# Optimization experiments

Hardware: AMD Instinct MI355X
Metric: run time of the kernel (lower is better)

Reference implementation:

```python
import math
import jax, jax.numpy as jnp
import numpy as np

B, S, D_IN, D_OUT = 8, 4096, 512, 512
CHUNK = 64
MAX_LR = 0.2        # config.max_memory_lr
MIN_DECAY = 0.5     # config.min_memory_decay
MAX_NORM = 30.0     # config.memory_max_norm
NORM_EPS = 1e-5     # config.norm_eps (used in normalize_for_delta)


def setup_inputs() -> dict:
    key = jax.random.key(0)
    ks = jax.random.split(key, 5)
    x = jax.random.normal(ks[0], (B, S, D_IN), dtype=jnp.float32)
    # M_init: xavier_uniform(gain=0.1) ~ small; use small normal
    M_init = jax.random.normal(ks[1], (D_OUT, D_IN), dtype=jnp.float32) * 0.02
    # hyperparam projections (Linear(d_in, 1)); torch init: zero weight, logit bias.
    # Use small random weights so the data-dependent path is exercised.
    eta_w = jax.random.normal(ks[2], (1, D_IN), dtype=jnp.float32) * 0.01
    eta_b = jnp.full((1,), math.log(0.08 / 0.92), dtype=jnp.float32)   # inv_sig(memory_lr_init)
    alpha_w = jax.random.normal(ks[3], (1, D_IN), dtype=jnp.float32) * 0.01
    alpha_b = jnp.full((1,), math.log(0.85 / 0.15), dtype=jnp.float32)  # inv_sig(memory_decay_init)
    gate_w = jax.random.normal(ks[4], (1, D_IN), dtype=jnp.float32) * 0.01
    gate_b = jnp.full((1,), 2.0, dtype=jnp.float32)
    return {"x": x, "M_init": M_init, "eta_w": eta_w, "eta_b": eta_b,
            "alpha_w": alpha_w, "alpha_b": alpha_b, "gate_w": gate_w, "gate_b": gate_b}


def _forward(x, M_init, eta_w, eta_b, alpha_w, alpha_b, gate_w, gate_b):
    n_chunks = S // CHUNK
    # [n_chunks, B, C, d_in] for scan over chunks
    xc = x.reshape(B, n_chunks, CHUNK, D_IN).transpose(1, 0, 2, 3)
    M0 = jnp.broadcast_to(M_init, (B, D_OUT, D_IN))

    def step(M, chunk):  # M: [B, d_out, d_in], chunk: [B, C, d_in]
        # per-chunk hyperparams (training mode: base logits = 0)
        eta_tok = jax.nn.sigmoid(chunk @ eta_w.T + eta_b) * MAX_LR            # [B,C,1]
        alpha_tok = MIN_DECAY + jax.nn.sigmoid(chunk @ alpha_w.T + alpha_b) * (1.0 - MIN_DECAY)
        eta = eta_tok.mean(axis=1, keepdims=True)    # [B,1,1]
        alpha = alpha_tok.mean(axis=1, keepdims=True)
        # retrieval: chunk @ M^T
        outputs = jnp.einsum('bcd,bod->bco', chunk, M)  # [B,C,d_out]
        # normalized keys (F.normalize: x / max(||x||, eps))
        kn = jnp.linalg.norm(chunk, axis=-1, keepdims=True)
        keys = chunk / jnp.maximum(kn, NORM_EPS)
        k_mean = keys.mean(axis=1)        # [B,d_in]
        v_target = outputs.mean(axis=1)   # [B,d_out]
        # delta rule rank-1 update
        Mk = jnp.einsum('bod,bd->bo', M, k_mean)
        error = v_target - Mk
        update = error[:, :, None] * k_mean[:, None, :]  # [B,d_out,d_in]
        # chunk_scale = min(C/chunk_size, 1) = 1 here
        M_new = alpha * M + eta * update
        gate = jax.nn.sigmoid(k_mean @ gate_w.T + gate_b)[:, :, None]  # [B,1,1]
        M_new = gate * M_new + (1.0 - gate) * M
        # frobenius-norm clamp
        M_norm = jnp.sqrt(jnp.sum(M_new * M_new, axis=(-2, -1), keepdims=True))
        scale = jnp.minimum(MAX_NORM / (M_norm + 1e-6), 1.0)
        return M_new * scale, outputs

    M_fin, outs = jax.lax.scan(step, M0, xc)  # outs: [n_chunks,B,C,d_out]
    out = outs.transpose(1, 0, 2, 3).reshape(B, S, D_OUT)
    return out, M_fin


def reference(x, M_init, eta_w, eta_b, alpha_w, alpha_b, gate_w, gate_b):
    return _forward(x, M_init, eta_w, eta_b, alpha_w, alpha_b, gate_w, gate_b)
```

## Files before the change

kernel.cpp:

```cpp
#include <hip/hip_runtime.h>
#include <math.h>

#define DIN  512
#define DOUT 512
#define CHK  64
#define NCH  64
#define NB   8
#define SEQ  4096

typedef short bh8_t __attribute__((ext_vector_type(8)));
typedef float f32x4 __attribute__((ext_vector_type(4)));

__device__ __forceinline__ float sigmoidf_(float z){ return 1.0f/(1.0f+__expf(-z)); }

__device__ __forceinline__ unsigned short f2bf(float f){
  unsigned u = __float_as_uint(f);
  unsigned r = (u + 0x7fffu + ((u>>16)&1u)) >> 16;
  return (unsigned short)r;
}
__device__ __forceinline__ void store_bf4(unsigned short* p, float4 v){
  uint2 u;
  u.x = (unsigned)f2bf(v.x) | ((unsigned)f2bf(v.y)<<16);
  u.y = (unsigned)f2bf(v.z) | ((unsigned)f2bf(v.w)<<16);
  *(uint2*)p = u;
}

__global__ __launch_bounds__(256) void k0_m0h(const float* __restrict__ M0, unsigned short* __restrict__ M0h){
  int idx = (blockIdx.x*256 + threadIdx.x)*4;
  float4 v = *(const float4*)(M0+idx);
  store_bf4(M0h+idx, v);
}

__global__ __launch_bounds__(256) void k1_stats(
    const float* __restrict__ x,
    const float* __restrict__ eta_w, const float* __restrict__ eta_b,
    const float* __restrict__ alpha_w, const float* __restrict__ alpha_b,
    const float* __restrict__ gate_w, const float* __restrict__ gate_b,
    float* __restrict__ KM, float* __restrict__ Dv, unsigned short* __restrict__ KMh,
    float* __restrict__ C1, float* __restrict__ C2, float* __restrict__ KM2, float* __restrict__ Q,
    unsigned short* __restrict__ xh)
{
  int j = blockIdx.x, b = blockIdx.y;
  const float* xc = x + ((size_t)b*SEQ + (size_t)j*CHK) * DIN;
  int tid = threadIdx.x;
  int wave = tid >> 6, lane = tid & 63;

  float km_acc[8], xb_acc[8];
#pragma unroll
  for (int k=0;k<8;k++){ km_acc[k]=0.f; xb_acc[k]=0.f; }
  float eta_sum = 0.f, alpha_sum = 0.f;
  float ew[8], aw[8];
#pragma unroll
  for (int k=0;k<8;k++){ ew[k]=eta_w[lane*8+k]; aw[k]=alpha_w[lane*8+k]; }

  for (int tt=0; tt<16; tt++){
    int t = wave*16 + tt;
    const float* xr = xc + (size_t)t*DIN + lane*8;
    float v[8];
#pragma unroll
    for (int k=0;k<8;k++) v[k]=xr[k];
    if (xh){
      uint4 hv;
      hv.x = (unsigned)f2bf(v[0]) | ((unsigned)f2bf(v[1])<<16);
      hv.y = (unsigned)f2bf(v[2]) | ((unsigned)f2bf(v[3])<<16);
      hv.z = (unsigned)f2bf(v[4]) | ((unsigned)f2bf(v[5])<<16);
      hv.w = (unsigned)f2bf(v[6]) | ((unsigned)f2bf(v[7])<<16);
      *(uint4*)&xh[((size_t)b*SEQ + (size_t)j*CHK + t)*DIN + lane*8] = hv;
    }
    float pe=0.f, pa=0.f, pn=0.f;
#pragma unroll
    for (int k=0;k<8;k++){ pe += v[k]*ew[k]; pa += v[k]*aw[k]; pn += v[k]*v[k]; }
#pragma unroll
    for (int off=32; off; off>>=1){
      pe += __shfl_xor(pe, off);
      pa += __shfl_xor(pa, off);
      pn += __shfl_xor(pn, off);
    }
    float inv = 1.0f / fmaxf(sqrtf(pn), 1e-5f);
    eta_sum   += sigmoidf_(pe + eta_b[0]);
    alpha_sum += sigmoidf_(pa + alpha_b[0]);
#pragma unroll
    for (int k=0;k<8;k++){ km_acc[k] += v[k]*inv; xb_acc[k] += v[k]; }
  }

  __shared__ float sKM[4][DIN];
  __shared__ float sXB[4][DIN];
  __shared__ float sEA[4][2];
  __shared__ float sred[4][2];
#pragma unroll
  for (int k=0;k<8;k++){ sKM[wave][lane*8+k]=km_acc[k]; sXB[wave][lane*8+k]=xb_acc[k]; }
  if (lane==0){ sEA[wave][0]=eta_sum; sEA[wave][1]=alpha_sum; }
  __syncthreads();

  float gpart=0.f, km2part=0.f;
  float kmv[2], dvv[2];
#pragma unroll
  for (int k=0;k<2;k++){
    int d = tid*2+k;
    float km = (sKM[0][d]+sKM[1][d]+sKM[2][d]+sKM[3][d]) * (1.0f/64.0f);
    float xb = (sXB[0][d]+sXB[1][d]+sXB[2][d]+sXB[3][d]) * (1.0f/64.0f);
    kmv[k]=km; dvv[k]=xb-km;
    gpart  += km * gate_w[d];
    km2part+= km * km;
  }
#pragma unroll
  for (int off=32; off; off>>=1){
    gpart   += __shfl_xor(gpart, off);
    km2part += __shfl_xor(km2part, off);
  }
  if (lane==0){ sred[wave][0]=gpart; sred[wave][1]=km2part; }
  __syncthreads();

  size_t base = ((size_t)b*NCH + j)*DIN;
#pragma unroll
  for (int k=0;k<2;k++){
    int d = tid*2+k;
    KM[base+d]=kmv[k];
    Dv[base+d]=dvv[k];
    KMh[base+d]=f2bf(kmv[k]);
  }
  if (tid==0){
    float gdot = sred[0][0]+sred[1][0]+sred[2][0]+sred[3][0];
    float km2  = sred[0][1]+sred[1][1]+sred[2][1]+sred[3][1];
    float etam = (sEA[0][0]+sEA[1][0]+sEA[2][0]+sEA[3][0]) * (1.0f/64.0f);
    float alpm = (sEA[0][1]+sEA[1][1]+sEA[2][1]+sEA[3][1]) * (1.0f/64.0f);
    float eta   = 0.2f * etam;
    float alpha = 0.5f + 0.5f * alpm;
    float gate  = sigmoidf_(gdot + gate_b[0]);
    float c1 = gate*alpha + 1.0f - gate;
    float c2 = gate*eta;
    C1[b*NCH+j]  = c1;
    C2[b*NCH+j]  = c2;
    KM2[b*NCH+j] = km2;
    Q[b*NCH+j]   = c2/c1;
  }
}

__global__ __launch_bounds__(256) void k2_g0h0(
    const float* __restrict__ KM, const float* __restrict__ Dv,
    const float* __restrict__ M0, float* __restrict__ G0, float* __restrict__ H0)
{
  int j = blockIdx.x, b = blockIdx.y;
  __shared__ float sD[DIN], sK[DIN];
  int tid = threadIdx.x;
  size_t base = ((size_t)b*NCH+j)*DIN;
  for (int d=tid; d<DIN; d+=256){ sD[d]=Dv[base+d]; sK[d]=KM[base+d]; }
  __syncthreads();
  for (int o=tid; o<DOUT; o+=256){
    const float* mr = M0 + (size_t)o*DIN;
    float ag=0.f, ah=0.f;
    for (int d=0; d<DIN; d+=4){
      float4 m = *(const float4*)(mr+d);
      ag += m.x*sD[d] + m.y*sD[d+1] + m.z*sD[d+2] + m.w*sD[d+3];
      ah += m.x*sK[d] + m.y*sK[d+1] + m.z*sK[d+2] + m.w*sK[d+3];
    }
    G0[base+o]=ag; H0[base+o]=ah;
  }
}

__global__ __launch_bounds__(256) void k2b_gram(
    const float* __restrict__ KM, const float* __restrict__ Dv,
    float* __restrict__ KMD, float* __restrict__ KMKM)
{
  int i = blockIdx.x, b = blockIdx.y;
  __shared__ float sKi[DIN];
  int tid = threadIdx.x;
  const float* kmi = KM + ((size_t)b*NCH+i)*DIN;
  for (int d=tid; d<DIN; d+=256) sKi[d]=kmi[d];
  __syncthreads();
  int wave = tid>>6, lane = tid&63;
  for (int j=wave; j<NCH; j+=4){
    const float* dj = Dv + ((size_t)b*NCH+j)*DIN;
    const float* kj = KM + ((size_t)b*NCH+j)*DIN;
    float pd=0.f, pk=0.f;
#pragma unroll
    for (int k=0;k<8;k++){
      int d = lane + k*64;
      pd += sKi[d]*dj[d];
      pk += sKi[d]*kj[d];
    }
#pragma unroll
    for (int off=32; off; off>>=1){ pd += __shfl_xor(pd,off); pk += __shfl_xor(pk,off); }
    if (lane==0){
      KMD [((size_t)b*NCH+i)*NCH + j] = pd;
      KMKM[((size_t)b*NCH+i)*NCH + j] = pk;
    }
  }
}

__global__ __launch_bounds__(256) void k3a_au(
    const float* __restrict__ G0, const float* __restrict__ H0,
    const float* __restrict__ KMD, const float* __restrict__ KMKM,
    const float* __restrict__ Q, float* __restrict__ AU,
    unsigned short* __restrict__ UQTh,
    float* __restrict__ DUW, float* __restrict__ DUU)
{
  int half = blockIdx.x, b = blockIdx.y;
  int tid = threadIdx.x, wave = tid>>6, lane = tid&63;
  int d = half*256 + tid;
  __shared__ float scM[4096], scW[4096];
  __shared__ float sq[64];
  __shared__ float sdots[64][4][2];

  for (int idx=tid; idx<4096; idx+=256){
    int i=idx>>6, jj=idx&63;
    float qv = Q[b*NCH+i];
    scM[idx] = qv*KMD [((size_t)b*NCH+i)*NCH+jj];
    scW[idx] = qv*KMKM[((size_t)b*NCH+i)*NCH+jj];
  }
  if (tid<64) sq[tid] = Q[b*NCH+tid];
  __syncthreads();

  float au[NCH];
  size_t gb = (size_t)b*NCH*DOUT + d;
#pragma unroll
  for (int j=0;j<NCH;j++) au[j] = G0[gb + (size_t)j*DOUT];

#pragma unroll
  for (int j=0;j<NCH;j++){
    float a = au[j];
#pragma unroll
    for (int i=0;i<j;i++) a += scM[i*64+j]*au[i];
    au[j]=a;
  }
#pragma unroll
  for (int j=0;j<NCH;j++) AU[gb + (size_t)j*DOUT] = au[j];

#pragma unroll
  for (int g=0; g<8; g++){
    uint4 hv;
    hv.x = (unsigned)f2bf(au[g*8+0]*sq[g*8+0]) | ((unsigned)f2bf(au[g*8+1]*sq[g*8+1])<<16);
    hv.y = (unsigned)f2bf(au[g*8+2]*sq[g*8+2]) | ((unsigned)f2bf(au[g*8+3]*sq[g*8+3])<<16);
    hv.z = (unsigned)f2bf(au[g*8+4]*sq[g*8+4]) | ((unsigned)f2bf(au[g*8+5]*sq[g*8+5])<<16);
    hv.w = (unsigned)f2bf(au[g*8+6]*sq[g*8+6]) | ((unsigned)f2bf(au[g*8+7]*sq[g*8+7])<<16);
    *(uint4*)&UQTh[((size_t)b*DOUT + d)*NCH + g*8] = hv;
  }

#pragma unroll
  for (int j=0;j<NCH;j++){
    float w = H0[gb + (size_t)j*DOUT];
#pragma unroll
    for (int i=0;i<j;i++) w += scW[i*64+j]*au[i];
    float s1 = au[j]*w, s2 = au[j]*au[j];
#pragma unroll
    for (int off=32; off; off>>=1){ s1+=__shfl_xor(s1,off); s2+=__shfl_xor(s2,off); }
    if (lane==0){ sdots[j][wave][0]=s1; sdots[j][wave][1]=s2; }
  }
  __syncthreads();
  if (tid<64){
    int j = tid;
    float uw = sdots[j][0][0]+sdots[j][1][0]+sdots[j][2][0]+sdots[j][3][0];
    float uu = sdots[j][0][1]+sdots[j][1][1]+sdots[j][2][1]+sdots[j][3][1];
    DUW[(b*NCH+j)*2 + half] = uw;
    DUU[(b*NCH+j)*2 + half] = uu;
  }
}

__global__ __launch_bounds__(256) void k3c_chain(
    const float* __restrict__ M0,
    const float* __restrict__ C1, const float* __restrict__ C2, const float* __restrict__ KM2,
    const float* __restrict__ DUW, const float* __restrict__ DUU, float* __restrict__ P)
{
  int b = blockIdx.x, tid = threadIdx.x, wave = tid>>6, lane = tid&63;
  float f=0.f;
  const float4* m4 = (const float4*)M0;
  for (int i=tid; i<(DOUT*DIN)/4; i+=256){
    float4 v=m4[i];
    f += v.x*v.x + v.y*v.y + v.z*v.z + v.w*v.w;
  }
#pragma unroll
  for (int off=32; off; off>>=1) f += __shfl_xor(f,off);
  __shared__ float rf[4];
  if (lane==0) rf[wave]=f;
  __syncthreads();
  if (tid==0){
    float F = rf[0]+rf[1]+rf[2]+rf[3];
    float p = 1.f;
    P[b*65+0] = 1.f;
    for (int j=0;j<NCH;j++){
      float c1 = C1[b*NCH+j], c2 = C2[b*NCH+j], km2 = KM2[b*NCH+j];
      float uw = p*p*(DUW[(b*NCH+j)*2]+DUW[(b*NCH+j)*2+1]);
      float uu = p*p*(DUU[(b*NCH+j)*2]+DUU[(b*NCH+j)*2+1]);
      float Fnew = c1*c1*F + 2.f*c1*c2*uw + c2*c2*uu*km2;
      float scale = fminf(30.0f/(sqrtf(Fnew)+1e-6f), 1.0f);
      F = scale*scale*Fnew;
      p = scale*c1*p;
      P[b*65+j+1] = p;
    }
  }
}

__global__ __launch_bounds__(256) void k4s_s(
    const float* __restrict__ x, const unsigned short* __restrict__ xh,
    const unsigned short* __restrict__ KMh,
    unsigned short* __restrict__ Sh, int use_xh)
{
  int tt = blockIdx.x, b = blockIdx.y;
  int tid = threadIdx.x;
  int lane = tid&63, w = tid>>6, m = lane&15, q = lane>>4;
  __shared__ unsigned short As[64*72];
  __shared__ unsigned short Bs[64*72];
  f32x4 acc[4];
  f32x4 z = {0.f,0.f,0.f,0.f};
#pragma unroll
  for (int nf=0;nf<4;nf++) acc[nf]=z;

  for (int k0=0;k0<DIN;k0+=64){
    uint4 bb[2];
#pragma unroll
    for (int v=0;v<2;v++){
      int idx=v*256+tid; int il=idx>>3, cc=idx&7;
      bb[v] = *(const uint4*)&KMh[((size_t)b*NCH+il)*DIN + k0 + cc*8];
    }
    if (use_xh){
      uint4 av[2];
#pragma unroll
      for (int v=0;v<2;v++){
        int idx=v*256+tid; int row=idx>>3, cc=idx&7;
        av[v] = *(const uint4*)&xh[((size_t)b*SEQ + (size_t)tt*64 + row)*DIN + k0 + cc*8];
      }
      __syncthreads();
#pragma unroll
      for (int v=0;v<2;v++){
        int idx=v*256+tid; int row=idx>>3, cc=idx&7;
        *(uint4*)&As[row*72 + cc*8] = av[v];
      }
    } else {
      float4 xa[4];
#pragma unroll
      for (int v=0;v<4;v++){
        int idx=v*256+tid; int row=idx>>4, cc=idx&15;
        xa[v] = *(const float4*)(x + ((size_t)b*SEQ + (size_t)tt*64 + row)*DIN + k0 + cc*4);
      }
      __syncthreads();
#pragma unroll
      for (int v=0;v<4;v++){
        int idx=v*256+tid; int row=idx>>4, cc=idx&15;
        store_bf4(&As[row*72 + cc*4], xa[v]);
      }
    }
#pragma unroll
    for (int v=0;v<2;v++){
      int idx=v*256+tid; int il=idx>>3, cc=idx&7;
      *(uint4*)&Bs[il*72 + cc*8] = bb[v];
    }
    __syncthreads();
#pragma unroll
    for (int kk=0;kk<2;kk++){
      bh8_t af = *(bh8_t*)&As[(w*16+m)*72 + kk*32 + q*8];
#pragma unroll
      for (int nf=0;nf<4;nf++){
        bh8_t bf_ = *(bh8_t*)&Bs[(nf*16+m)*72 + kk*32 + q*8];
        acc[nf] = __builtin_amdgcn_mfma_f32_16x16x32_bf16(af, bf_, acc[nf], 0,0,0);
      }
    }
  }
#pragma unroll
  for (int nf=0;nf<4;nf++)
#pragma unroll
    for (int r=0;r<4;r++)
      Sh[((size_t)b*SEQ + (size_t)tt*64 + w*16 + q*4 + r)*NCH + nf*16 + m] = f2bf(acc[nf][r]);
}

__global__ __launch_bounds__(256) void k4_out(
    const float* __restrict__ x, const unsigned short* __restrict__ xh,
    const unsigned short* __restrict__ M0h,
    const unsigned short* __restrict__ Sh, const unsigned short* __restrict__ UQTh,
    const float* __restrict__ P, float* __restrict__ out, int use_xh)
{
  int ot = blockIdx.x, j = blockIdx.y, b = blockIdx.z;
  int tid = threadIdx.x;
  int lane = tid&63, w = tid>>6, m = lane&15, q = lane>>4;
  int O0 = ot*256;
  __shared__ unsigned short As[64*72];
  __shared__ unsigned short Bs[256*72];
  f32x4 acc[16];
  f32x4 z = {0.f,0.f,0.f,0.f};
#pragma unroll
  for (int nf=0;nf<16;nf++) acc[nf]=z;

  for (int idx=tid; idx<64*64; idx+=256){
    int t = idx>>6, i = idx&63;
    As[t*72+i] = (i<j) ? Sh[((size_t)b*SEQ + (size_t)j*64 + t)*NCH + i] : (unsigned short)0;
  }
#pragma unroll
  for (int v=0; v<8; v++){
    int idx = v*256+tid;
    int ol = idx>>3, cc = idx&7;
    *(uint4*)&Bs[ol*72 + cc*8] = *(const uint4*)&UQTh[((size_t)b*DOUT + O0+ol)*NCH + cc*8];
  }
  __syncthreads();
#pragma unroll
  for (int kk=0;kk<2;kk++){
    bh8_t af = *(bh8_t*)&As[(w*16+m)*72 + kk*32 + q*8];
#pragma unroll
    for (int nf=0;nf<16;nf++){
      bh8_t bf_ = *(bh8_t*)&Bs[(nf*16+m)*72 + kk*32 + q*8];
      acc[nf] = __builtin_amdgcn_mfma_f32_16x16x32_bf16(af, bf_, acc[nf], 0,0,0);
    }
  }

  for (int k0=0;k0<DIN;k0+=64){
    uint4 bb[8];
#pragma unroll
    for (int v=0;v<8;v++){
      int idx=v*256+tid; int ol=idx>>3, cc=idx&7;
      bb[v] = *(const uint4*)&M0h[(size_t)(O0+ol)*DIN + k0 + cc*8];
    }
    if (use_xh){
      uint4 av[2];
#pragma unroll
      for (int v=0;v<2;v++){
        int idx=v*256+tid; int row=idx>>3, cc=idx&7;
        av[v] = *(const uint4*)&xh[((size_t)b*SEQ + (size_t)j*64 + row)*DIN + k0 + cc*8];
      }
      __syncthreads();
#pragma unroll
      for (int v=0;v<2;v++){
        int idx=v*256+tid; int row=idx>>3, cc=idx&7;
        *(uint4*)&As[row*72 + cc*8] = av[v];
      }
    } else {
      float4 xa[4];
#pragma unroll
      for (int v=0;v<4;v++){
        int idx=v*256+tid; int row=idx>>4, cc=idx&15;
        xa[v] = *(const float4*)(x + ((size_t)b*SEQ + (size_t)j*64 + row)*DIN + k0 + cc*4);
      }
      __syncthreads();
#pragma unroll
      for (int v=0;v<4;v++){
        int idx=v*256+tid; int row=idx>>4, cc=idx&15;
        store_bf4(&As[row*72 + cc*4], xa[v]);
      }
    }
#pragma unroll
    for (int v=0;v<8;v++){
      int idx=v*256+tid; int ol=idx>>3, cc=idx&7;
      *(uint4*)&Bs[ol*72 + cc*8] = bb[v];
    }
    __syncthreads();
#pragma unroll
    for (int kk=0;kk<2;kk++){
      bh8_t af = *(bh8_t*)&As[(w*16+m)*72 + kk*32 + q*8];
#pragma unroll
      for (int nf=0;nf<16;nf++){
        bh8_t bf_ = *(bh8_t*)&Bs[(nf*16+m)*72 + kk*32 + q*8];
        acc[nf] = __builtin_amdgcn_mfma_f32_16x16x32_bf16(af, bf_, acc[nf], 0,0,0);
      }
    }
  }

  float p = P[b*65 + j];
#pragma unroll
  for (int nf=0;nf<16;nf++)
#pragma unroll
    for (int r=0;r<4;r++)
      out[((size_t)b*SEQ + (size_t)j*64 + w*16 + q*4 + r)*DOUT + O0 + nf*16 + m] = p*acc[nf][r];
}

__global__ __launch_bounds__(256) void k5_mfin(
    const float* __restrict__ M0, const float* __restrict__ KM,
    const float* __restrict__ AU, const float* __restrict__ P, const float* __restrict__ Q,
    float* __restrict__ Mout)
{
  int ob = blockIdx.x, b = blockIdx.y;
  int tid = threadIdx.x;
  __shared__ float uo[64][8];
  for (int idx=tid; idx<512; idx+=256){
    int i = idx>>3, oo = idx&7;
    uo[i][oo] = Q[b*NCH+i] * AU[((size_t)b*NCH+i)*DOUT + ob*8+oo];
  }
  __syncthreads();
  float p64 = P[b*65+NCH];
  float acc[2][8];
#pragma unroll
  for (int h=0;h<2;h++)
#pragma unroll
    for (int oo=0;oo<8;oo++) acc[h][oo]=0.f;
  int d0 = tid, d1 = tid+256;
  for (int i=0;i<64;i++){
    float k0 = KM[((size_t)b*NCH+i)*DIN + d0];
    float k1 = KM[((size_t)b*NCH+i)*DIN + d1];
#pragma unroll
    for (int oo=0;oo<8;oo++){
      float u = uo[i][oo];
      acc[0][oo] += u*k0;
      acc[1][oo] += u*k1;
    }
  }
#pragma unroll
  for (int oo=0;oo<8;oo++){
    int o = ob*8+oo;
    Mout[((size_t)b*DOUT + o)*DIN + d0] = p64*(M0[(size_t)o*DIN+d0] + acc[0][oo]);
    Mout[((size_t)b*DOUT + o)*DIN + d1] = p64*(M0[(size_t)o*DIN+d1] + acc[1][oo]);
  }
}

extern "C" void kernel_launch(void* const* d_in, const int* in_sizes, int n_in,
                              void* d_out, int out_size, void* d_ws, size_t ws_size,
                              hipStream_t stream) {
  const float* x       = (const float*)d_in[0];
  const float* M0      = (const float*)d_in[1];
  const float* eta_w   = (const float*)d_in[2];
  const float* eta_b   = (const float*)d_in[3];
  const float* alpha_w = (const float*)d_in[4];
  const float* alpha_b = (const float*)d_in[5];
  const float* gate_w  = (const float*)d_in[6];
  const float* gate_b  = (const float*)d_in[7];
  float* out = (float*)d_out;

  float* ws = (float*)d_ws;
  float* KM   = ws;
  float* Dv   = KM   + 262144;
  float* G0   = Dv   + 262144;
  float* H0   = G0   + 262144;
  float* AU   = H0   + 262144;
  float* KMD  = AU   + 262144;
  float* KMKM = KMD  + 32768;
  float* C1   = KMKM + 32768;
  float* C2   = C1   + 512;
  float* KM2  = C2   + 512;
  float* Q    = KM2  + 512;
  float* DUW  = Q    + 512;
  float* DUU  = DUW  + 1024;
  float* P    = DUU  + 1024;
  unsigned short* M0h  = (unsigned short*)(P + 1024);
  unsigned short* KMh  = M0h  + 262144;
  unsigned short* Sh   = KMh  + 262144;
  unsigned short* UQTh = Sh   + 2097152;
  unsigned short* xh   = UQTh + 262144;

  size_t base_bytes = (size_t)((char*)xh - (char*)d_ws);
  size_t need_xh = base_bytes + (size_t)16777216*2;
  int use_xh = (ws_size >= need_xh) ? 1 : 0;
  unsigned short* xh_arg = use_xh ? xh : (unsigned short*)0;

  k0_m0h<<<dim3(256), 256, 0, stream>>>(M0, M0h);
  k1_stats<<<dim3(NCH, NB), 256, 0, stream>>>(x, eta_w, eta_b, alpha_w, alpha_b,
                                              gate_w, gate_b, KM, Dv, KMh, C1, C2, KM2, Q, xh_arg);
  k2_g0h0<<<dim3(NCH, NB), 256, 0, stream>>>(KM, Dv, M0, G0, H0);
  k2b_gram<<<dim3(NCH, NB), 256, 0, stream>>>(KM, Dv, KMD, KMKM);
  k4s_s<<<dim3(SEQ/64, NB), 256, 0, stream>>>(x, xh, KMh, Sh, use_xh);
  k3a_au<<<dim3(2, NB), 256, 0, stream>>>(G0, H0, KMD, KMKM, Q, AU, UQTh, DUW, DUU);
  k3c_chain<<<dim3(NB), 256, 0, stream>>>(M0, C1, C2, KM2, DUW, DUU, P);
  k4_out<<<dim3(2, NCH, NB), 256, 0, stream>>>(x, xh, M0h, Sh, UQTh, P, out, use_xh);
  k5_mfin<<<dim3(64, NB), 256, 0, stream>>>(M0, KM, AU, P, Q, out + (size_t)NB*SEQ*DOUT);
}
```

Measured before the change: 511.4 us.

## Fuse triangular solve with norm chain, split GEMM tiles, stage stores via LDS

The AU triangular solve and the scalar norm-chain kernel are merged into one 512-thread block per batch, which drops the DUW/DUU round trip and one launch. k2_g0h0 gets twice as many blocks (one per output half), and k2b_gram moves to 512 threads. k4_out halves its output tile to 128 columns so the grid doubles, and it stages results through LDS for coalesced float4 stores; k4s_s stages its bf16 stores the same way. The risk is that fewer blocks in the fused solve lengthen that serial step, and the smaller output tiles reload the A operand more often.

```diff
diff --git a/kernel.cpp b/kernel.cpp
--- a/kernel.cpp
+++ b/kernel.cpp
@@ -140,25 +140,24 @@
     const float* __restrict__ KM, const float* __restrict__ Dv,
     const float* __restrict__ M0, float* __restrict__ G0, float* __restrict__ H0)
 {
-  int j = blockIdx.x, b = blockIdx.y;
+  int j = blockIdx.x, b = blockIdx.y, half = blockIdx.z;
   __shared__ float sD[DIN], sK[DIN];
   int tid = threadIdx.x;
   size_t base = ((size_t)b*NCH+j)*DIN;
   for (int d=tid; d<DIN; d+=256){ sD[d]=Dv[base+d]; sK[d]=KM[base+d]; }
   __syncthreads();
-  for (int o=tid; o<DOUT; o+=256){
-    const float* mr = M0 + (size_t)o*DIN;
-    float ag=0.f, ah=0.f;
-    for (int d=0; d<DIN; d+=4){
-      float4 m = *(const float4*)(mr+d);
-      ag += m.x*sD[d] + m.y*sD[d+1] + m.z*sD[d+2] + m.w*sD[d+3];
-      ah += m.x*sK[d] + m.y*sK[d+1] + m.z*sK[d+2] + m.w*sK[d+3];
-    }
-    G0[base+o]=ag; H0[base+o]=ah;
-  }
-}
-
-__global__ __launch_bounds__(256) void k2b_gram(
+  int o = half*256 + tid;
+  const float* mr = M0 + (size_t)o*DIN;
+  float ag=0.f, ah=0.f;
+  for (int d=0; d<DIN; d+=4){
+    float4 m = *(const float4*)(mr+d);
+    ag += m.x*sD[d] + m.y*sD[d+1] + m.z*sD[d+2] + m.w*sD[d+3];
+    ah += m.x*sK[d] + m.y*sK[d+1] + m.z*sK[d+2] + m.w*sK[d+3];
+  }
+  G0[base+o]=ag; H0[base+o]=ah;
+}
+
+__global__ __launch_bounds__(512) void k2b_gram(
     const float* __restrict__ KM, const float* __restrict__ Dv,
     float* __restrict__ KMD, float* __restrict__ KMKM)
 {
@@ -166,10 +165,10 @@
   __shared__ float sKi[DIN];
   int tid = threadIdx.x;
   const float* kmi = KM + ((size_t)b*NCH+i)*DIN;
-  for (int d=tid; d<DIN; d+=256) sKi[d]=kmi[d];
+  for (int d=tid; d<DIN; d+=512) sKi[d]=kmi[d];
   __syncthreads();
   int wave = tid>>6, lane = tid&63;
-  for (int j=wave; j<NCH; j+=4){
+  for (int j=wave; j<NCH; j+=8){
     const float* dj = Dv + ((size_t)b*NCH+j)*DIN;
     const float* kj = KM + ((size_t)b*NCH+j)*DIN;
     float pd=0.f, pk=0.f;
@@ -188,31 +187,42 @@
   }
 }
 
-__global__ __launch_bounds__(256) void k3a_au(
+__global__ __launch_bounds__(512) void k3_fused(
+    const float* __restrict__ M0,
     const float* __restrict__ G0, const float* __restrict__ H0,
     const float* __restrict__ KMD, const float* __restrict__ KMKM,
-    const float* __restrict__ Q, float* __restrict__ AU,
-    unsigned short* __restrict__ UQTh,
-    float* __restrict__ DUW, float* __restrict__ DUU)
-{
-  int half = blockIdx.x, b = blockIdx.y;
+    const float* __restrict__ Q,
+    const float* __restrict__ C1, const float* __restrict__ C2, const float* __restrict__ KM2,
+    float* __restrict__ AU, unsigned short* __restrict__ UQTh, float* __restrict__ P)
+{
+  int b = blockIdx.x;
   int tid = threadIdx.x, wave = tid>>6, lane = tid&63;
-  int d = half*256 + tid;
   __shared__ float scM[4096], scW[4096];
   __shared__ float sq[64];
-  __shared__ float sdots[64][4][2];
-
-  for (int idx=tid; idx<4096; idx+=256){
+  __shared__ float sdots[64][8][2];
+  __shared__ float sred[8];
+
+  for (int idx=tid; idx<4096; idx+=512){
     int i=idx>>6, jj=idx&63;
     float qv = Q[b*NCH+i];
     scM[idx] = qv*KMD [((size_t)b*NCH+i)*NCH+jj];
     scW[idx] = qv*KMKM[((size_t)b*NCH+i)*NCH+jj];
   }
   if (tid<64) sq[tid] = Q[b*NCH+tid];
+
+  float f0p = 0.f;
+  const float4* m4 = (const float4*)M0;
+  for (int i=tid; i<(DOUT*DIN)/4; i+=512){
+    float4 v = m4[i];
+    f0p += v.x*v.x + v.y*v.y + v.z*v.z + v.w*v.w;
+  }
+#pragma unroll
+  for (int off=32; off; off>>=1) f0p += __shfl_xor(f0p, off);
+  if (lane==0) sred[wave]=f0p;
   __syncthreads();
 
   float au[NCH];
-  size_t gb = (size_t)b*NCH*DOUT + d;
+  size_t gb = (size_t)b*NCH*DOUT + tid;
 #pragma unroll
   for (int j=0;j<NCH;j++) au[j] = G0[gb + (size_t)j*DOUT];
 
@@ -233,7 +243,7 @@
     hv.y = (unsigned)f2bf(au[g*8+2]*sq[g*8+2]) | ((unsigned)f2bf(au[g*8+3]*sq[g*8+3])<<16);
     hv.z = (unsigned)f2bf(au[g*8+4]*sq[g*8+4]) | ((unsigned)f2bf(au[g*8+5]*sq[g*8+5])<<16);
     hv.w = (unsigned)f2bf(au[g*8+6]*sq[g*8+6]) | ((unsigned)f2bf(au[g*8+7]*sq[g*8+7])<<16);
-    *(uint4*)&UQTh[((size_t)b*DOUT + d)*NCH + g*8] = hv;
+    *(uint4*)&UQTh[((size_t)b*DOUT + tid)*NCH + g*8] = hv;
   }
 
 #pragma unroll
@@ -247,40 +257,19 @@
     if (lane==0){ sdots[j][wave][0]=s1; sdots[j][wave][1]=s2; }
   }
   __syncthreads();
-  if (tid<64){
-    int j = tid;
-    float uw = sdots[j][0][0]+sdots[j][1][0]+sdots[j][2][0]+sdots[j][3][0];
-    float uu = sdots[j][0][1]+sdots[j][1][1]+sdots[j][2][1]+sdots[j][3][1];
-    DUW[(b*NCH+j)*2 + half] = uw;
-    DUU[(b*NCH+j)*2 + half] = uu;
-  }
-}
-
-__global__ __launch_bounds__(256) void k3c_chain(
-    const float* __restrict__ M0,
-    const float* __restrict__ C1, const float* __restrict__ C2, const float* __restrict__ KM2,
-    const float* __restrict__ DUW, const float* __restrict__ DUU, float* __restrict__ P)
-{
-  int b = blockIdx.x, tid = threadIdx.x, wave = tid>>6, lane = tid&63;
-  float f=0.f;
-  const float4* m4 = (const float4*)M0;
-  for (int i=tid; i<(DOUT*DIN)/4; i+=256){
-    float4 v=m4[i];
-    f += v.x*v.x + v.y*v.y + v.z*v.z + v.w*v.w;
-  }
-#pragma unroll
-  for (int off=32; off; off>>=1) f += __shfl_xor(f,off);
-  __shared__ float rf[4];
-  if (lane==0) rf[wave]=f;
-  __syncthreads();
+
   if (tid==0){
-    float F = rf[0]+rf[1]+rf[2]+rf[3];
+    float F = 0.f;
+#pragma unroll
+    for (int w2=0;w2<8;w2++) F += sred[w2];
     float p = 1.f;
     P[b*65+0] = 1.f;
     for (int j=0;j<NCH;j++){
+      float uw=0.f, uu=0.f;
+#pragma unroll
+      for (int w2=0;w2<8;w2++){ uw += sdots[j][w2][0]; uu += sdots[j][w2][1]; }
       float c1 = C1[b*NCH+j], c2 = C2[b*NCH+j], km2 = KM2[b*NCH+j];
-      float uw = p*p*(DUW[(b*NCH+j)*2]+DUW[(b*NCH+j)*2+1]);
-      float uu = p*p*(DUU[(b*NCH+j)*2]+DUU[(b*NCH+j)*2+1]);
+      uw *= p*p; uu *= p*p;
       float Fnew = c1*c1*F + 2.f*c1*c2*uw + c2*c2*uu*km2;
       float scale = fminf(30.0f/(sqrtf(Fnew)+1e-6f), 1.0f);
       F = scale*scale*Fnew;
@@ -355,11 +344,20 @@
       }
     }
   }
+  __syncthreads();
+  unsigned short* tb = As + w*16*72;
 #pragma unroll
   for (int nf=0;nf<4;nf++)
 #pragma unroll
     for (int r=0;r<4;r++)
-      Sh[((size_t)b*SEQ + (size_t)tt*64 + w*16 + q*4 + r)*NCH + nf*16 + m] = f2bf(acc[nf][r]);
+      tb[(q*4+r)*72 + nf*16 + m] = f2bf(acc[nf][r]);
+#pragma unroll
+  for (int v=0;v<2;v++){
+    int idx = v*64 + lane;
+    int row = idx>>3, c8 = idx&7;
+    uint4 vv = *(uint4*)&tb[row*72 + c8*8];
+    *(uint4*)&Sh[((size_t)b*SEQ + (size_t)tt*64 + w*16 + row)*NCH + c8*8] = vv;
+  }
 }
 
 __global__ __launch_bounds__(256) void k4_out(
@@ -371,20 +369,23 @@
   int ot = blockIdx.x, j = blockIdx.y, b = blockIdx.z;
   int tid = threadIdx.x;
   int lane = tid&63, w = tid>>6, m = lane&15, q = lane>>4;
-  int O0 = ot*256;
-  __shared__ unsigned short As[64*72];
-  __shared__ unsigned short Bs[256*72];
-  f32x4 acc[16];
+  int O0 = ot*128;
+  __shared__ __align__(16) char pool[33792];
+  unsigned short* As = (unsigned short*)pool;
+  unsigned short* Bs = (unsigned short*)pool + 64*72;
+  float* ep = (float*)pool;
+  f32x4 acc[8];
   f32x4 z = {0.f,0.f,0.f,0.f};
 #pragma unroll
-  for (int nf=0;nf<16;nf++) acc[nf]=z;
+  for (int nf=0;nf<8;nf++) acc[nf]=z;
+  float p = P[b*65 + j];
 
   for (int idx=tid; idx<64*64; idx+=256){
     int t = idx>>6, i = idx&63;
     As[t*72+i] = (i<j) ? Sh[((size_t)b*SEQ + (size_t)j*64 + t)*NCH + i] : (unsigned short)0;
   }
 #pragma unroll
-  for (int v=0; v<8; v++){
+  for (int v=0; v<4; v++){
     int idx = v*256+tid;
     int ol = idx>>3, cc = idx&7;
     *(uint4*)&Bs[ol*72 + cc*8] = *(const uint4*)&UQTh[((size_t)b*DOUT + O0+ol)*NCH + cc*8];
@@ -394,16 +395,16 @@
   for (int kk=0;kk<2;kk++){
     bh8_t af = *(bh8_t*)&As[(w*16+m)*72 + kk*32 + q*8];
 #pragma unroll
-    for (int nf=0;nf<16;nf++){
+    for (int nf=0;nf<8;nf++){
       bh8_t bf_ = *(bh8_t*)&Bs[(nf*16+m)*72 + kk*32 + q*8];
       acc[nf] = __builtin_amdgcn_mfma_f32_16x16x32_bf16(af, bf_, acc[nf], 0,0,0);
     }
   }
 
   for (int k0=0;k0<DIN;k0+=64){
-    uint4 bb[8];
-#pragma unroll
-    for (int v=0;v<8;v++){
+    uint4 bb[4];
+#pragma unroll
+    for (int v=0;v<4;v++){
       int idx=v*256+tid; int ol=idx>>3, cc=idx&7;
       bb[v] = *(const uint4*)&M0h[(size_t)(O0+ol)*DIN + k0 + cc*8];
     }
@@ -435,7 +436,7 @@
       }
     }
 #pragma unroll
-    for (int v=0;v<8;v++){
+    for (int v=0;v<4;v++){
       int idx=v*256+tid; int ol=idx>>3, cc=idx&7;
       *(uint4*)&Bs[ol*72 + cc*8] = bb[v];
     }
@@ -444,19 +445,27 @@
     for (int kk=0;kk<2;kk++){
       bh8_t af = *(bh8_t*)&As[(w*16+m)*72 + kk*32 + q*8];
 #pragma unroll
-      for (int nf=0;nf<16;nf++){
+      for (int nf=0;nf<8;nf++){
         bh8_t bf_ = *(bh8_t*)&Bs[(nf*16+m)*72 + kk*32 + q*8];
         acc[nf] = __builtin_amdgcn_mfma_f32_16x16x32_bf16(af, bf_, acc[nf], 0,0,0);
       }
     }
   }
 
-  float p = P[b*65 + j];
-#pragma unroll
-  for (int nf=0;nf<16;nf++)
+  __syncthreads();
+  float* epw = ep + w*16*132;
+#pragma unroll
+  for (int nf=0;nf<8;nf++)
 #pragma unroll
     for (int r=0;r<4;r++)
-      out[((size_t)b*SEQ + (size_t)j*64 + w*16 + q*4 + r)*DOUT + O0 + nf*16 + m] = p*acc[nf][r];
+      epw[(q*4+r)*132 + nf*16 + m] = p*acc[nf][r];
+#pragma unroll
+  for (int v=0;v<8;v++){
+    int idx = v*64 + lane;
+    int row = idx>>5, c4 = idx&31;
+    float4 vv = *(float4*)&epw[row*132 + c4*4];
+    *(float4*)&out[((size_t)b*SEQ + (size_t)j*64 + w*16 + row)*DOUT + O0 + c4*4] = vv;
+  }
 }
 
 __global__ __launch_bounds__(256) void k5_mfin(
@@ -522,9 +531,7 @@
   float* C2   = C1   + 512;
   float* KM2  = C2   + 512;
   float* Q    = KM2  + 512;
-  float* DUW  = Q    + 512;
-  float* DUU  = DUW  + 1024;
-  float* P    = DUU  + 1024;
+  float* P    = Q    + 512;
   unsigned short* M0h  = (unsigned short*)(P + 1024);
   unsigned short* KMh  = M0h  + 262144;
   unsigned short* Sh   = KMh  + 262144;
@@ -539,11 +546,10 @@
   k0_m0h<<<dim3(256), 256, 0, stream>>>(M0, M0h);
   k1_stats<<<dim3(NCH, NB), 256, 0, stream>>>(x, eta_w, eta_b, alpha_w, alpha_b,
                                               gate_w, gate_b, KM, Dv, KMh, C1, C2, KM2, Q, xh_arg);
-  k2_g0h0<<<dim3(NCH, NB), 256, 0, stream>>>(KM, Dv, M0, G0, H0);
-  k2b_gram<<<dim3(NCH, NB), 256, 0, stream>>>(KM, Dv, KMD, KMKM);
+  k2_g0h0<<<dim3(NCH, NB, 2), 256, 0, stream>>>(KM, Dv, M0, G0, H0);
+  k2b_gram<<<dim3(NCH, NB), 512, 0, stream>>>(KM, Dv, KMD, KMKM);
   k4s_s<<<dim3(SEQ/64, NB), 256, 0, stream>>>(x, xh, KMh, Sh, use_xh);
-  k3a_au<<<dim3(2, NB), 256, 0, stream>>>(G0, H0, KMD, KMKM, Q, AU, UQTh, DUW, DUU);
-  k3c_chain<<<dim3(NB), 256, 0, stream>>>(M0, C1, C2, KM2, DUW, DUU, P);
-  k4_out<<<dim3(2, NCH, NB), 256, 0, stream>>>(x, xh, M0h, Sh, UQTh, P, out, use_xh);
+  k3_fused<<<dim3(NB), 512, 0, stream>>>(M0, G0, H0, KMD, KMKM, Q, C1, C2, KM2, AU, UQTh, P);
+  k4_out<<<dim3(4, NCH, NB), 256, 0, stream>>>(x, xh, M0h, Sh, UQTh, P, out, use_xh);
   k5_mfin<<<dim3(64, NB), 256, 0, stream>>>(M0, KM, AU, P, Q, out + (size_t)NB*SEQ*DOUT);
 }
```

New measurement: 494.1 us. 1.04x faster.
